# Performance work log

Hardware: AMD Instinct MI355X
Metric: run time of the kernel (lower is better)

## Reference

```python
import jax, jax.numpy as jnp
import numpy as np

BN_EPS = 1e-5
B, L, D = 16, 2048, 1024
OS = 64          # attnList[0]
NC = 256         # candidates per sample
CLASS_NUM = 8921
LAB = 1024


def setup_inputs() -> dict:
    key = jax.random.key(0)
    ks = jax.random.split(key, 8)
    scale_a = 1.0 / np.sqrt(D)
    return {
        "X": jax.random.normal(ks[0], (B, L, D), jnp.float32),
        "candidate": jax.random.randint(ks[1], (B, NC), 0, CLASS_NUM, jnp.int64),
        "a_w": jax.random.normal(ks[2], (D, OS), jnp.float32) * scale_a,
        "a_b": jnp.zeros((OS,), jnp.float32),
        "h_w": jax.random.normal(ks[3], (D, LAB), jnp.float32) * scale_a,
        "h_b": jnp.zeros((LAB,), jnp.float32),
        "bn_gamma": jax.random.uniform(ks[4], (LAB,), jnp.float32, 0.5, 1.5),
        "bn_beta": jax.random.normal(ks[5], (LAB,), jnp.float32) * 0.1,
        "bn_mean": jnp.zeros((LAB,), jnp.float32),
        "bn_var": jnp.ones((LAB,), jnp.float32),
        "labDescVec": jax.random.normal(ks[6], (CLASS_NUM, LAB), jnp.float32),
    }


def reference(X, candidate, a_w, a_b, h_w, h_b, bn_gamma, bn_beta, bn_mean, bn_var, labDescVec):
    # --- attention-pooling layer (attnList has one entry) ---
    # alpha: softmax over the sequence dim (dim=1 in torch)
    alpha = jax.nn.softmax(jnp.einsum('bld,do->blo', X, a_w) + a_b, axis=1)  # [B,L,OS]
    Xp = jnp.einsum('blo,bld->bod', alpha, X)                                # [B,OS,D]
    Xp = jnp.einsum('bod,dh->boh', Xp, h_w) + h_b                            # [B,OS,LAB]
    # BatchNorm1d over feature dim (eval mode: running stats)
    Xp = (Xp - bn_mean) * (bn_gamma / jnp.sqrt(bn_var + BN_EPS)) + bn_beta
    Xp = jax.nn.relu(Xp)  # dropout is identity at inference
    # --- candidate attention ---
    batchLabelVec = labDescVec[candidate]                                    # [B,NC,LAB]
    scores = jnp.einsum('boh,bch->boc', Xp, batchLabelVec)                   # [B,OS,NC]
    alpha2 = jax.nn.softmax(scores, axis=1)                                  # softmax over OS (dim=1)
    out = jnp.einsum('boc,boh->bch', alpha2, Xp)                             # [B,NC,LAB]
    return out
```

## Files before the change

kernel.cpp:

```cpp
#include <hip/hip_runtime.h>
#include <math.h>

#define Bb   16
#define Ll   2048
#define Dd   1024
#define OSo  64
#define NCc  256
#define LABh 1024
#define BN_EPS 1e-5f

typedef short s8v  __attribute__((ext_vector_type(8)));
typedef short s4v  __attribute__((ext_vector_type(4)));
typedef float f32x4 __attribute__((ext_vector_type(4)));

__device__ __forceinline__ short f2b(float f) {
    union { float f; unsigned u; } v; v.f = f;
    unsigned r = (v.u + 0x7fffu + ((v.u >> 16) & 1u)) >> 16;
    return (short)r;
}
__device__ __forceinline__ float b2f(short s) {
    union { unsigned u; float f; } v; v.u = ((unsigned)(unsigned short)s) << 16;
    return v.f;
}
__device__ __forceinline__ int swi(int row, int kElem) {
    return (row * 128 + ((kElem * 2) ^ ((row & 7) << 4))) >> 1;
}
__device__ __forceinline__ f32x4 MF(s8v a, s8v b, f32x4 c) {
    return __builtin_amdgcn_mfma_f32_16x16x32_bf16(a, b, c, 0, 0, 0);
}

__global__ __launch_bounds__(256) void k0(const float* __restrict__ h_w,
                                          const float* __restrict__ a_w,
                                          short* __restrict__ h_wT,
                                          short* __restrict__ a_wT) {
    __shared__ float t[64][68];
    const int tid = threadIdx.x, id = blockIdx.x;
    const float* src; short* dst; int srw, d0, y0;
    if (id < 256) { src = h_w; dst = h_wT; srw = LABh; d0 = (id & 15) * 64; y0 = (id >> 4) * 64; }
    else          { src = a_w; dst = a_wT; srw = OSo;  d0 = (id - 256) * 64; y0 = 0; }
    const int r = tid >> 2, cofs = (tid & 3) * 16;
    #pragma unroll
    for (int w = 0; w < 4; ++w) {
        float4 v = *(const float4*)&src[(size_t)(d0 + r) * srw + y0 + cofs + w * 4];
        t[r][cofs + w * 4 + 0] = v.x;
        t[r][cofs + w * 4 + 1] = v.y;
        t[r][cofs + w * 4 + 2] = v.z;
        t[r][cofs + w * 4 + 3] = v.w;
    }
    __syncthreads();
    s8v o0, o1;
    #pragma unroll
    for (int e = 0; e < 8; ++e) { o0[e] = f2b(t[cofs + e][r]); o1[e] = f2b(t[cofs + 8 + e][r]); }
    *(s8v*)&dst[(size_t)(y0 + r) * Dd + d0 + cofs]     = o0;
    *(s8v*)&dst[(size_t)(y0 + r) * Dd + d0 + cofs + 8] = o1;
}

struct R1 { float4 x[4]; s8v w[2]; };

__global__ __launch_bounds__(256) void k1(const float* __restrict__ X,
                                          const short* __restrict__ a_wT,
                                          const float* __restrict__ a_b,
                                          float* __restrict__ St) {
    __shared__ __align__(16) char smem[32768];
    float (*ts)[65] = (float(*)[65])smem;
    const int tid = threadIdx.x;
    const int lane = tid & 63, wave = tid >> 6;
    const int wm = wave >> 1, wn = wave & 1;
    const int b = blockIdx.y, l0 = blockIdx.x * 64;
    const float* Xb = X + ((size_t)b * Ll + l0) * Dd;
    const int r = tid >> 2, kofs = (tid & 3) * 16;
    f32x4 acc[2][2] = {};
    R1 cur, nxt;
    #pragma unroll
    for (int w = 0; w < 2; ++w) {
        cur.x[2*w]   = *(const float4*)&Xb[(size_t)r * Dd + kofs + w * 8];
        cur.x[2*w+1] = *(const float4*)&Xb[(size_t)r * Dd + kofs + w * 8 + 4];
        cur.w[w]     = *(const s8v*)&a_wT[(size_t)r * Dd + kofs + w * 8];
    }
    #pragma unroll
    for (int t = 0; t < 16; ++t) {
        short* As = (short*)(smem + (t & 1) * 8192);
        short* Bs = (short*)(smem + 16384 + (t & 1) * 8192);
        #pragma unroll
        for (int w = 0; w < 2; ++w) {
            const float* f0 = (const float*)&cur.x[2*w];
            s8v s;
            s[0]=f2b(f0[0]); s[1]=f2b(f0[1]); s[2]=f2b(f0[2]); s[3]=f2b(f0[3]);
            s[4]=f2b(f0[4]); s[5]=f2b(f0[5]); s[6]=f2b(f0[6]); s[7]=f2b(f0[7]);
            *(s8v*)&As[swi(r, kofs + w * 8)] = s;
            *(s8v*)&Bs[swi(r, kofs + w * 8)] = cur.w[w];
        }
        __syncthreads();
        if (t < 15) {
            const int k0 = (t + 1) * 64;
            #pragma unroll
            for (int w = 0; w < 2; ++w) {
                nxt.x[2*w]   = *(const float4*)&Xb[(size_t)r * Dd + k0 + kofs + w * 8];
                nxt.x[2*w+1] = *(const float4*)&Xb[(size_t)r * Dd + k0 + kofs + w * 8 + 4];
                nxt.w[w]     = *(const s8v*)&a_wT[(size_t)r * Dd + k0 + kofs + w * 8];
            }
        }
        #pragma unroll
        for (int kk = 0; kk < 2; ++kk) {
            const int kb = kk * 32 + (lane >> 4) * 8;
            s8v a[2], bb[2];
            #pragma unroll
            for (int i = 0; i < 2; ++i)
                a[i] = *(const s8v*)&As[swi(wm * 32 + i * 16 + (lane & 15), kb)];
            #pragma unroll
            for (int j = 0; j < 2; ++j)
                bb[j] = *(const s8v*)&Bs[swi(wn * 32 + j * 16 + (lane & 15), kb)];
            #pragma unroll
            for (int i = 0; i < 2; ++i)
                #pragma unroll
                for (int j = 0; j < 2; ++j)
                    acc[i][j] = MF(a[i], bb[j], acc[i][j]);
        }
        if (t < 15) cur = nxt;
    }
    __syncthreads();
    #pragma unroll
    for (int i = 0; i < 2; ++i)
        #pragma unroll
        for (int j = 0; j < 2; ++j)
            #pragma unroll
            for (int rr = 0; rr < 4; ++rr)
                ts[wm * 32 + i * 16 + (lane >> 4) * 4 + rr][wn * 32 + j * 16 + (lane & 15)] = acc[i][j][rr];
    __syncthreads();
    const int o = tid >> 2, lofs = (tid & 3) * 16;
    const float bias = a_b[o];
    float* Sp = St + ((size_t)b * OSo + o) * Ll + l0 + lofs;
    #pragma unroll
    for (int w = 0; w < 4; ++w) {
        float4 v;
        v.x = ts[lofs + w * 4 + 0][o] + bias;
        v.y = ts[lofs + w * 4 + 1][o] + bias;
        v.z = ts[lofs + w * 4 + 2][o] + bias;
        v.w = ts[lofs + w * 4 + 3][o] + bias;
        *(float4*)&Sp[w * 4] = v;
    }
}

__global__ __launch_bounds__(256) void k2(const float* __restrict__ St, short* __restrict__ aBf) {
    __shared__ float row[Ll];
    __shared__ float red[8];
    const float* p = St + (size_t)blockIdx.x * Ll;
    short* ab = aBf + (size_t)blockIdx.x * Ll;
    const int tid = threadIdx.x;
    const int wave = tid >> 6, lane = tid & 63;
    float m = -1e30f;
    for (int i = tid; i < Ll; i += 256) { float v = p[i]; row[i] = v; m = fmaxf(m, v); }
    #pragma unroll
    for (int off = 32; off; off >>= 1) m = fmaxf(m, __shfl_down(m, off));
    if (lane == 0) red[wave] = m;
    __syncthreads();
    if (tid == 0) red[4] = fmaxf(fmaxf(red[0], red[1]), fmaxf(red[2], red[3]));
    __syncthreads();
    const float M = red[4];
    float s = 0.f;
    for (int i = tid; i < Ll; i += 256) { float e = __expf(row[i] - M); row[i] = e; s += e; }
    __syncthreads();
    #pragma unroll
    for (int off = 32; off; off >>= 1) s += __shfl_down(s, off);
    if (lane == 0) red[wave] = s;
    __syncthreads();
    if (tid == 0) red[4] = 1.f / (red[0] + red[1] + red[2] + red[3]);
    __syncthreads();
    const float inv = red[4];
    for (int i = tid; i < Ll; i += 256) ab[i] = f2b(row[i] * inv);
}

struct R3 { s8v al[2]; float4 xv[4]; };

__global__ __launch_bounds__(256) void k3(const float* __restrict__ X,
                                          const short* __restrict__ aBf,
                                          float* __restrict__ XpP) {
    __shared__ __align__(16) char smem[32768];
    float (*ts)[68] = (float(*)[68])smem;
    const int tid = threadIdx.x;
    const int lane = tid & 63, wave = tid >> 6;
    const int wm = wave >> 1, wn = wave & 1;
    const int id = blockIdx.x;
    const int slot = id >> 3;
    const int b = (id & 7) * 2 + (slot >> 5);
    const int inner = slot & 31;
    const int dt = inner & 15, z = inner >> 4;
    const int d0 = dt * 64;
    const float* Xb = X + (size_t)b * Ll * Dd;
    const short* ab = aBf + (size_t)b * OSo * Ll;
    float* outP = XpP + (size_t)z * ((size_t)Bb * OSo * Dd);
    f32x4 acc[2][2] = {};
    const int arow = tid >> 2, akofs = (tid & 3) * 16;
    const int lq = tid & 15, dq = tid >> 4;
    const int lbase = z * 1024;
    R3 cur, nxt;
    #pragma unroll
    for (int w = 0; w < 2; ++w)
        cur.al[w] = *(const s8v*)&ab[(size_t)arow * Ll + lbase + akofs + w * 8];
    #pragma unroll
    for (int i = 0; i < 4; ++i)
        cur.xv[i] = *(const float4*)&Xb[(size_t)(lbase + lq * 4 + i) * Dd + d0 + dq * 4];
    #pragma unroll
    for (int t = 0; t < 16; ++t) {
        short* Aal = (short*)(smem + (t & 1) * 8192);
        short* Xs  = (short*)(smem + 16384 + (t & 1) * 8192);
        #pragma unroll
        for (int w = 0; w < 2; ++w)
            *(s8v*)&Aal[swi(arow, akofs + w * 8)] = cur.al[w];
        {
            const float* f = (const float*)cur.xv;
            #pragma unroll
            for (int j = 0; j < 4; ++j) {
                const int rowd = dq * 4 + j;
                s4v sj;
                sj[0] = f2b(f[0 * 4 + j]);
                sj[1] = f2b(f[1 * 4 + j]);
                sj[2] = f2b(f[2 * 4 + j]);
                sj[3] = f2b(f[3 * 4 + j]);
                *(s4v*)&Xs[swi(rowd, lq * 4)] = sj;
            }
        }
        __syncthreads();
        if (t < 15) {
            const int l0 = lbase + (t + 1) * 64;
            #pragma unroll
            for (int w = 0; w < 2; ++w)
                nxt.al[w] = *(const s8v*)&ab[(size_t)arow * Ll + l0 + akofs + w * 8];
            #pragma unroll
            for (int i = 0; i < 4; ++i)
                nxt.xv[i] = *(const float4*)&Xb[(size_t)(l0 + lq * 4 + i) * Dd + d0 + dq * 4];
        }
        #pragma unroll
        for (int kk = 0; kk < 2; ++kk) {
            const int kb = kk * 32 + (lane >> 4) * 8;
            s8v a[2], bb[2];
            #pragma unroll
            for (int i = 0; i < 2; ++i)
                a[i] = *(const s8v*)&Aal[swi(wm * 32 + i * 16 + (lane & 15), kb)];
            #pragma unroll
            for (int j = 0; j < 2; ++j)
                bb[j] = *(const s8v*)&Xs[swi(wn * 32 + j * 16 + (lane & 15), kb)];
            #pragma unroll
            for (int i = 0; i < 2; ++i)
                #pragma unroll
                for (int j = 0; j < 2; ++j)
                    acc[i][j] = MF(a[i], bb[j], acc[i][j]);
        }
        if (t < 15) cur = nxt;
    }
    __syncthreads();
    #pragma unroll
    for (int i = 0; i < 2; ++i)
        #pragma unroll
        for (int j = 0; j < 2; ++j)
            #pragma unroll
            for (int rr = 0; rr < 4; ++rr)
                ts[wm * 32 + i * 16 + (lane >> 4) * 4 + rr][wn * 32 + j * 16 + (lane & 15)] = acc[i][j][rr];
    __syncthreads();
    const int o = tid >> 2, dofs = (tid & 3) * 16;
    float* op = outP + ((size_t)b * OSo + o) * Dd + d0 + dofs;
    #pragma unroll
    for (int w = 0; w < 4; ++w)
        *(float4*)&op[w * 4] = *(float4*)&ts[o][dofs + w * 4];
}

struct R4 { float4 p[8]; s8v w[2]; };

__global__ __launch_bounds__(256) void k4(const float* __restrict__ XpP,
                                          const short* __restrict__ h_wT,
                                          const float* __restrict__ h_b,
                                          const float* __restrict__ gamma,
                                          const float* __restrict__ beta,
                                          const float* __restrict__ mean,
                                          const float* __restrict__ var,
                                          short* __restrict__ Xh) {
    __shared__ __align__(16) char smem[32768];
    short* tsb = (short*)smem;
    const int tid = threadIdx.x, lane = tid & 63, wave = tid >> 6;
    const int wm = wave >> 1, wn = wave & 1;
    const int h0 = blockIdx.x * 64, m0 = blockIdx.y * 64;
    const int r = tid >> 2, kofs = (tid & 3) * 16;
    const size_t ZS = (size_t)Bb * OSo * Dd;
    f32x4 acc[2][2] = {};
    R4 cur, nxt;
    #pragma unroll
    for (int w = 0; w < 2; ++w) {
        const float* p0 = XpP + (size_t)(m0 + r) * Dd + kofs + w * 8;
        cur.p[w*4+0] = *(const float4*)&p0[0];
        cur.p[w*4+1] = *(const float4*)&p0[4];
        cur.p[w*4+2] = *(const float4*)&p0[ZS];
        cur.p[w*4+3] = *(const float4*)&p0[ZS + 4];
        cur.w[w]     = *(const s8v*)&h_wT[(size_t)(h0 + r) * Dd + kofs + w * 8];
    }
    #pragma unroll
    for (int t = 0; t < 16; ++t) {
        short* As = (short*)(smem + (t & 1) * 8192);
        short* Bs = (short*)(smem + 16384 + (t & 1) * 8192);
        #pragma unroll
        for (int w = 0; w < 2; ++w) {
            const float* f0 = (const float*)&cur.p[w*4];
            const float* f1 = (const float*)&cur.p[w*4+2];
            s8v s;
            #pragma unroll
            for (int e = 0; e < 8; ++e) s[e] = f2b(f0[e] + f1[e]);
            *(s8v*)&As[swi(r, kofs + w * 8)] = s;
            *(s8v*)&Bs[swi(r, kofs + w * 8)] = cur.w[w];
        }
        __syncthreads();
        if (t < 15) {
            const int k0 = (t + 1) * 64;
            #pragma unroll
            for (int w = 0; w < 2; ++w) {
                const float* p0 = XpP + (size_t)(m0 + r) * Dd + k0 + kofs + w * 8;
                nxt.p[w*4+0] = *(const float4*)&p0[0];
                nxt.p[w*4+1] = *(const float4*)&p0[4];
                nxt.p[w*4+2] = *(const float4*)&p0[ZS];
                nxt.p[w*4+3] = *(const float4*)&p0[ZS + 4];
                nxt.w[w]     = *(const s8v*)&h_wT[(size_t)(h0 + r) * Dd + k0 + kofs + w * 8];
            }
        }
        #pragma unroll
        for (int kk = 0; kk < 2; ++kk) {
            const int kb = kk * 32 + (lane >> 4) * 8;
            s8v a[2], bb[2];
            #pragma unroll
            for (int i = 0; i < 2; ++i)
                a[i] = *(const s8v*)&As[swi(wm * 32 + i * 16 + (lane & 15), kb)];
            #pragma unroll
            for (int j = 0; j < 2; ++j)
                bb[j] = *(const s8v*)&Bs[swi(wn * 32 + j * 16 + (lane & 15), kb)];
            #pragma unroll
            for (int i = 0; i < 2; ++i)
                #pragma unroll
                for (int j = 0; j < 2; ++j)
                    acc[i][j] = MF(a[i], bb[j], acc[i][j]);
        }
        if (t < 15) cur = nxt;
    }
    __syncthreads();
    #pragma unroll
    for (int j = 0; j < 2; ++j) {
        const int h = h0 + wn * 32 + j * 16 + (lane & 15);
        const float sc = gamma[h] * rsqrtf(var[h] + BN_EPS);
        const float of = (h_b[h] - mean[h]) * sc + beta[h];
        #pragma unroll
        for (int i = 0; i < 2; ++i)
            #pragma unroll
            for (int rr = 0; rr < 4; ++rr) {
                const int ml = wm * 32 + i * 16 + (lane >> 4) * 4 + rr;
                tsb[ml * 64 + wn * 32 + j * 16 + (lane & 15)] = f2b(fmaxf(0.f, acc[i][j][rr] * sc + of));
            }
    }
    __syncthreads();
    #pragma unroll
    for (int w = 0; w < 2; ++w)
        *(s8v*)&Xh[(size_t)(m0 + r) * LABh + h0 + kofs + w * 8] = *(const s8v*)&tsb[r * 64 + kofs + w * 8];
}

struct R5 { float4 ld[4]; s8v xh[2]; };

__global__ __launch_bounds__(256) void k5(const int* __restrict__ cand,
                                          const float* __restrict__ labD,
                                          const short* __restrict__ Xh,
                                          float* __restrict__ scP) {
    __shared__ __align__(16) char smem[33024];
    float (*ts)[68] = (float(*)[68])smem;
    int* cidx = (int*)(smem + 32768);
    const int tid = threadIdx.x, lane = tid & 63, wave = tid >> 6;
    const int wm = wave >> 1, wn = wave & 1;
    const int b = blockIdx.y;
    const int ct = blockIdx.x & 3, z = blockIdx.x >> 2;
    const int c0 = ct * 64;
    const int kbase = z * 256;
    if (tid < 64) cidx[tid] = cand[b * NCc + c0 + tid];
    __syncthreads();
    const int r = tid >> 2, kofs = (tid & 3) * 16;
    const int ci = cidx[r];
    const float* lrow = labD + (size_t)ci * LABh + kbase;
    const short* xrow = Xh + (size_t)(b * OSo + r) * LABh + kbase;
    f32x4 acc[2][2] = {};
    R5 cur, nxt;
    #pragma unroll
    for (int w = 0; w < 2; ++w) {
        cur.ld[2*w]   = *(const float4*)&lrow[kofs + w * 8];
        cur.ld[2*w+1] = *(const float4*)&lrow[kofs + w * 8 + 4];
        cur.xh[w]     = *(const s8v*)&xrow[kofs + w * 8];
    }
    #pragma unroll
    for (int t = 0; t < 4; ++t) {
        short* As = (short*)(smem + (t & 1) * 8192);
        short* Bs = (short*)(smem + 16384 + (t & 1) * 8192);
        #pragma unroll
        for (int w = 0; w < 2; ++w) {
            const float* f0 = (const float*)&cur.ld[2*w];
            s8v s;
            #pragma unroll
            for (int e = 0; e < 8; ++e) s[e] = f2b(f0[e]);
            *(s8v*)&As[swi(r, kofs + w * 8)] = s;
            *(s8v*)&Bs[swi(r, kofs + w * 8)] = cur.xh[w];
        }
        __syncthreads();
        if (t < 3) {
            const int k0 = (t + 1) * 64;
            #pragma unroll
            for (int w = 0; w < 2; ++w) {
                cur.ld[2*w];
                nxt.ld[2*w]   = *(const float4*)&lrow[k0 + kofs + w * 8];
                nxt.ld[2*w+1] = *(const float4*)&lrow[k0 + kofs + w * 8 + 4];
                nxt.xh[w]     = *(const s8v*)&xrow[k0 + kofs + w * 8];
            }
        }
        #pragma unroll
        for (int kk = 0; kk < 2; ++kk) {
            const int kb = kk * 32 + (lane >> 4) * 8;
            s8v a[2], bb[2];
            #pragma unroll
            for (int i = 0; i < 2; ++i)
                a[i] = *(const s8v*)&As[swi(wm * 32 + i * 16 + (lane & 15), kb)];
            #pragma unroll
            for (int j = 0; j < 2; ++j)
                bb[j] = *(const s8v*)&Bs[swi(wn * 32 + j * 16 + (lane & 15), kb)];
            #pragma unroll
            for (int i = 0; i < 2; ++i)
                #pragma unroll
                for (int j = 0; j < 2; ++j)
                    acc[i][j] = MF(a[i], bb[j], acc[i][j]);
        }
        if (t < 3) cur = nxt;
    }
    __syncthreads();
    #pragma unroll
    for (int i = 0; i < 2; ++i)
        #pragma unroll
        for (int j = 0; j < 2; ++j)
            #pragma unroll
            for (int rr = 0; rr < 4; ++rr)
                ts[wm * 32 + i * 16 + (lane >> 4) * 4 + rr][wn * 32 + j * 16 + (lane & 15)] = acc[i][j][rr];
    __syncthreads();
    const int oofs = (tid & 3) * 16;
    float* sp = scP + (size_t)z * ((size_t)Bb * NCc * OSo)
                    + ((size_t)b * NCc + c0 + r) * OSo + oofs;
    #pragma unroll
    for (int w = 0; w < 4; ++w)
        *(float4*)&sp[w * 4] = *(float4*)&ts[r][oofs + w * 4];
}

__global__ __launch_bounds__(256) void k6(const float* __restrict__ scP,
                                          const short* __restrict__ Xh,
                                          float* __restrict__ out) {
    __shared__ float al[16][64];
    const int tid = threadIdx.x;
    const int id = blockIdx.x;
    const int b = (id & 7) * 2 + ((id >> 3) >> 4);
    const int c0 = ((id >> 3) & 15) * 16;
    const size_t ZS = (size_t)Bb * NCc * OSo;
    {
        const int cl = tid >> 4, t16 = tid & 15;
        const float* srow = scP + ((size_t)b * NCc + c0 + cl) * OSo;
        float v[4];
        float m = -1e30f;
        #pragma unroll
        for (int j = 0; j < 4; ++j) {
            v[j] = srow[t16 + j * 16] + srow[ZS + t16 + j * 16]
                 + srow[2 * ZS + t16 + j * 16] + srow[3 * ZS + t16 + j * 16];
            m = fmaxf(m, v[j]);
        }
        #pragma unroll
        for (int off = 8; off; off >>= 1) m = fmaxf(m, __shfl_xor(m, off, 16));
        float s = 0.f;
        #pragma unroll
        for (int j = 0; j < 4; ++j) { v[j] = __expf(v[j] - m); s += v[j]; }
        #pragma unroll
        for (int off = 8; off; off >>= 1) s += __shfl_xor(s, off, 16);
        float inv = 1.f / s;
        #pragma unroll
        for (int j = 0; j < 4; ++j) al[cl][t16 + j * 16] = v[j] * inv;
    }
    __syncthreads();
    const short* xb = Xh + (size_t)b * OSo * LABh;
    float acc[16][4] = {};
    for (int o = 0; o < OSo; ++o) {
        s4v xv = *(const s4v*)&xb[(size_t)o * LABh + tid * 4];
        const float x0 = b2f(xv[0]), x1 = b2f(xv[1]), x2 = b2f(xv[2]), x3 = b2f(xv[3]);
        #pragma unroll
        for (int c = 0; c < 16; ++c) {
            const float w = al[c][o];
            acc[c][0] += w * x0; acc[c][1] += w * x1; acc[c][2] += w * x2; acc[c][3] += w * x3;
        }
    }
    #pragma unroll
    for (int c = 0; c < 16; ++c) {
        float4 v; v.x = acc[c][0]; v.y = acc[c][1]; v.z = acc[c][2]; v.w = acc[c][3];
        *(float4*)&out[((size_t)b * NCc + c0 + c) * LABh + tid * 4] = v;
    }
}

extern "C" void kernel_launch(void* const* d_in, const int* in_sizes, int n_in,
                              void* d_out, int out_size, void* d_ws, size_t ws_size,
                              hipStream_t stream) {
    (void)in_sizes; (void)n_in; (void)out_size; (void)ws_size;
    const float* X      = (const float*)d_in[0];
    const int*   cand   = (const int*)  d_in[1];
    const float* a_w    = (const float*)d_in[2];
    const float* a_b    = (const float*)d_in[3];
    const float* h_w    = (const float*)d_in[4];
    const float* h_b    = (const float*)d_in[5];
    const float* gamma  = (const float*)d_in[6];
    const float* beta   = (const float*)d_in[7];
    const float* mean   = (const float*)d_in[8];
    const float* var    = (const float*)d_in[9];
    const float* labDesc= (const float*)d_in[10];
    float* outp = (float*)d_out;

    char* ws = (char*)d_ws;
    float* St   = (float*)ws;
    float* XpP  = St;
    short* aBf  = (short*)(ws + ((size_t)8  << 20));
    short* Xh   = (short*)(ws + ((size_t)12 << 20));
    float* scP  = (float*)(ws + ((size_t)14 << 20));
    short* a_wT = (short*)(ws + ((size_t)18 << 20));
    short* h_wT = (short*)(ws + ((size_t)19 << 20));

    k0 <<<272,          256, 0, stream>>>(h_w, a_w, h_wT, a_wT);
    k1 <<<dim3(32, 16), 256, 0, stream>>>(X, a_wT, a_b, St);
    k2 <<<Bb * OSo,     256, 0, stream>>>(St, aBf);
    k3 <<<512,          256, 0, stream>>>(X, aBf, XpP);
    k4 <<<dim3(16, 16), 256, 0, stream>>>(XpP, h_wT, h_b, gamma, beta, mean, var, Xh);
    k5 <<<dim3(16, 16), 256, 0, stream>>>(cand, labDesc, Xh, scP);
    k6 <<<256,          256, 0, stream>>>(scP, Xh, outp);
}
```

Before: 112.0 us.

## Split k1 over K, emit bf16 X copy for k3, double k6 grid

k1 is split into two K halves across blockIdx.z, producing partial scores that k2 sums along with the bias. While converting X to bf16 for its MFMA, k1 also writes that bf16 copy to workspace, so k3 reads half the bytes and skips its own conversion. k6 now uses 8 candidates per block and 512 blocks for more parallelism. The trade is an extra 64MB bf16 write plus a second partial-score buffer in exchange for halving k3's read traffic.

```diff
diff --git a/kernel.cpp b/kernel.cpp
--- a/kernel.cpp
+++ b/kernel.cpp
@@ -59,26 +59,29 @@
 
 __global__ __launch_bounds__(256) void k1(const float* __restrict__ X,
                                           const short* __restrict__ a_wT,
-                                          const float* __restrict__ a_b,
-                                          float* __restrict__ St) {
+                                          float* __restrict__ StP,
+                                          short* __restrict__ Xbf) {
     __shared__ __align__(16) char smem[32768];
     float (*ts)[65] = (float(*)[65])smem;
     const int tid = threadIdx.x;
     const int lane = tid & 63, wave = tid >> 6;
     const int wm = wave >> 1, wn = wave & 1;
     const int b = blockIdx.y, l0 = blockIdx.x * 64;
+    const int z = blockIdx.z, kbase = z * 512;
     const float* Xb = X + ((size_t)b * Ll + l0) * Dd;
+    short* XbfRow = Xbf + ((size_t)b * Ll + l0) * Dd;
     const int r = tid >> 2, kofs = (tid & 3) * 16;
     f32x4 acc[2][2] = {};
     R1 cur, nxt;
     #pragma unroll
     for (int w = 0; w < 2; ++w) {
-        cur.x[2*w]   = *(const float4*)&Xb[(size_t)r * Dd + kofs + w * 8];
-        cur.x[2*w+1] = *(const float4*)&Xb[(size_t)r * Dd + kofs + w * 8 + 4];
-        cur.w[w]     = *(const s8v*)&a_wT[(size_t)r * Dd + kofs + w * 8];
-    }
-    #pragma unroll
-    for (int t = 0; t < 16; ++t) {
+        cur.x[2*w]   = *(const float4*)&Xb[(size_t)r * Dd + kbase + kofs + w * 8];
+        cur.x[2*w+1] = *(const float4*)&Xb[(size_t)r * Dd + kbase + kofs + w * 8 + 4];
+        cur.w[w]     = *(const s8v*)&a_wT[(size_t)r * Dd + kbase + kofs + w * 8];
+    }
+    #pragma unroll
+    for (int t = 0; t < 8; ++t) {
+        const int k0 = kbase + t * 64;
         short* As = (short*)(smem + (t & 1) * 8192);
         short* Bs = (short*)(smem + 16384 + (t & 1) * 8192);
         #pragma unroll
@@ -89,15 +92,16 @@
             s[4]=f2b(f0[4]); s[5]=f2b(f0[5]); s[6]=f2b(f0[6]); s[7]=f2b(f0[7]);
             *(s8v*)&As[swi(r, kofs + w * 8)] = s;
             *(s8v*)&Bs[swi(r, kofs + w * 8)] = cur.w[w];
+            *(s8v*)&XbfRow[(size_t)r * Dd + k0 + kofs + w * 8] = s;
         }
         __syncthreads();
-        if (t < 15) {
-            const int k0 = (t + 1) * 64;
+        if (t < 7) {
+            const int kn = k0 + 64;
             #pragma unroll
             for (int w = 0; w < 2; ++w) {
-                nxt.x[2*w]   = *(const float4*)&Xb[(size_t)r * Dd + k0 + kofs + w * 8];
-                nxt.x[2*w+1] = *(const float4*)&Xb[(size_t)r * Dd + k0 + kofs + w * 8 + 4];
-                nxt.w[w]     = *(const s8v*)&a_wT[(size_t)r * Dd + k0 + kofs + w * 8];
+                nxt.x[2*w]   = *(const float4*)&Xb[(size_t)r * Dd + kn + kofs + w * 8];
+                nxt.x[2*w+1] = *(const float4*)&Xb[(size_t)r * Dd + kn + kofs + w * 8 + 4];
+                nxt.w[w]     = *(const s8v*)&a_wT[(size_t)r * Dd + kn + kofs + w * 8];
             }
         }
         #pragma unroll
@@ -116,7 +120,7 @@
                 for (int j = 0; j < 2; ++j)
                     acc[i][j] = MF(a[i], bb[j], acc[i][j]);
         }
-        if (t < 15) cur = nxt;
+        if (t < 7) cur = nxt;
     }
     __syncthreads();
     #pragma unroll
@@ -128,28 +132,36 @@
                 ts[wm * 32 + i * 16 + (lane >> 4) * 4 + rr][wn * 32 + j * 16 + (lane & 15)] = acc[i][j][rr];
     __syncthreads();
     const int o = tid >> 2, lofs = (tid & 3) * 16;
-    const float bias = a_b[o];
-    float* Sp = St + ((size_t)b * OSo + o) * Ll + l0 + lofs;
+    float* Sp = StP + (size_t)z * ((size_t)Bb * OSo * Ll)
+                    + ((size_t)b * OSo + o) * Ll + l0 + lofs;
     #pragma unroll
     for (int w = 0; w < 4; ++w) {
         float4 v;
-        v.x = ts[lofs + w * 4 + 0][o] + bias;
-        v.y = ts[lofs + w * 4 + 1][o] + bias;
-        v.z = ts[lofs + w * 4 + 2][o] + bias;
-        v.w = ts[lofs + w * 4 + 3][o] + bias;
+        v.x = ts[lofs + w * 4 + 0][o];
+        v.y = ts[lofs + w * 4 + 1][o];
+        v.z = ts[lofs + w * 4 + 2][o];
+        v.w = ts[lofs + w * 4 + 3][o];
         *(float4*)&Sp[w * 4] = v;
     }
 }
 
-__global__ __launch_bounds__(256) void k2(const float* __restrict__ St, short* __restrict__ aBf) {
+__global__ __launch_bounds__(256) void k2(const float* __restrict__ StP,
+                                          const float* __restrict__ a_b,
+                                          short* __restrict__ aBf) {
     __shared__ float row[Ll];
     __shared__ float red[8];
-    const float* p = St + (size_t)blockIdx.x * Ll;
+    const size_t ZS = (size_t)Bb * OSo * Ll;
+    const float* p0 = StP + (size_t)blockIdx.x * Ll;
+    const float* p1 = p0 + ZS;
     short* ab = aBf + (size_t)blockIdx.x * Ll;
     const int tid = threadIdx.x;
     const int wave = tid >> 6, lane = tid & 63;
+    const float bias = a_b[blockIdx.x & (OSo - 1)];
     float m = -1e30f;
-    for (int i = tid; i < Ll; i += 256) { float v = p[i]; row[i] = v; m = fmaxf(m, v); }
+    for (int i = tid; i < Ll; i += 256) {
+        float v = p0[i] + p1[i] + bias;
+        row[i] = v; m = fmaxf(m, v);
+    }
     #pragma unroll
     for (int off = 32; off; off >>= 1) m = fmaxf(m, __shfl_down(m, off));
     if (lane == 0) red[wave] = m;
@@ -170,9 +182,9 @@
     for (int i = tid; i < Ll; i += 256) ab[i] = f2b(row[i] * inv);
 }
 
-struct R3 { s8v al[2]; float4 xv[4]; };
-
-__global__ __launch_bounds__(256) void k3(const float* __restrict__ X,
+struct R3 { s8v al[2]; s4v xv[4]; };
+
+__global__ __launch_bounds__(256) void k3(const short* __restrict__ Xbf,
                                           const short* __restrict__ aBf,
                                           float* __restrict__ XpP) {
     __shared__ __align__(16) char smem[32768];
@@ -186,7 +198,7 @@
     const int inner = slot & 31;
     const int dt = inner & 15, z = inner >> 4;
     const int d0 = dt * 64;
-    const float* Xb = X + (size_t)b * Ll * Dd;
+    const short* Xb = Xbf + (size_t)b * Ll * Dd;
     const short* ab = aBf + (size_t)b * OSo * Ll;
     float* outP = XpP + (size_t)z * ((size_t)Bb * OSo * Dd);
     f32x4 acc[2][2] = {};
@@ -199,7 +211,7 @@
         cur.al[w] = *(const s8v*)&ab[(size_t)arow * Ll + lbase + akofs + w * 8];
     #pragma unroll
     for (int i = 0; i < 4; ++i)
-        cur.xv[i] = *(const float4*)&Xb[(size_t)(lbase + lq * 4 + i) * Dd + d0 + dq * 4];
+        cur.xv[i] = *(const s4v*)&Xb[(size_t)(lbase + lq * 4 + i) * Dd + d0 + dq * 4];
     #pragma unroll
     for (int t = 0; t < 16; ++t) {
         short* Aal = (short*)(smem + (t & 1) * 8192);
@@ -207,18 +219,15 @@
         #pragma unroll
         for (int w = 0; w < 2; ++w)
             *(s8v*)&Aal[swi(arow, akofs + w * 8)] = cur.al[w];
-        {
-            const float* f = (const float*)cur.xv;
-            #pragma unroll
-            for (int j = 0; j < 4; ++j) {
-                const int rowd = dq * 4 + j;
-                s4v sj;
-                sj[0] = f2b(f[0 * 4 + j]);
-                sj[1] = f2b(f[1 * 4 + j]);
-                sj[2] = f2b(f[2 * 4 + j]);
-                sj[3] = f2b(f[3 * 4 + j]);
-                *(s4v*)&Xs[swi(rowd, lq * 4)] = sj;
-            }
+        #pragma unroll
+        for (int j = 0; j < 4; ++j) {
+            const int rowd = dq * 4 + j;
+            s4v sj;
+            sj[0] = cur.xv[0][j];
+            sj[1] = cur.xv[1][j];
+            sj[2] = cur.xv[2][j];
+            sj[3] = cur.xv[3][j];
+            *(s4v*)&Xs[swi(rowd, lq * 4)] = sj;
         }
         __syncthreads();
         if (t < 15) {
@@ -228,7 +237,7 @@
                 nxt.al[w] = *(const s8v*)&ab[(size_t)arow * Ll + l0 + akofs + w * 8];
             #pragma unroll
             for (int i = 0; i < 4; ++i)
-                nxt.xv[i] = *(const float4*)&Xb[(size_t)(l0 + lq * 4 + i) * Dd + d0 + dq * 4];
+                nxt.xv[i] = *(const s4v*)&Xb[(size_t)(l0 + lq * 4 + i) * Dd + d0 + dq * 4];
         }
         #pragma unroll
         for (int kk = 0; kk < 2; ++kk) {
@@ -404,7 +413,6 @@
             const int k0 = (t + 1) * 64;
             #pragma unroll
             for (int w = 0; w < 2; ++w) {
-                cur.ld[2*w];
                 nxt.ld[2*w]   = *(const float4*)&lrow[k0 + kofs + w * 8];
                 nxt.ld[2*w+1] = *(const float4*)&lrow[k0 + kofs + w * 8 + 4];
                 nxt.xh[w]     = *(const s8v*)&xrow[k0 + kofs + w * 8];
@@ -448,48 +456,49 @@
 __global__ __launch_bounds__(256) void k6(const float* __restrict__ scP,
                                           const short* __restrict__ Xh,
                                           float* __restrict__ out) {
-    __shared__ float al[16][64];
+    __shared__ float al[8][64];
     const int tid = threadIdx.x;
     const int id = blockIdx.x;
-    const int b = (id & 7) * 2 + ((id >> 3) >> 4);
-    const int c0 = ((id >> 3) & 15) * 16;
+    const int slot = id >> 3;
+    const int b = (id & 7) * 2 + (slot >> 5);
+    const int c0 = (slot & 31) * 8;
     const size_t ZS = (size_t)Bb * NCc * OSo;
     {
-        const int cl = tid >> 4, t16 = tid & 15;
+        const int cl = tid >> 5, t32 = tid & 31;
         const float* srow = scP + ((size_t)b * NCc + c0 + cl) * OSo;
-        float v[4];
+        float v[2];
         float m = -1e30f;
         #pragma unroll
-        for (int j = 0; j < 4; ++j) {
-            v[j] = srow[t16 + j * 16] + srow[ZS + t16 + j * 16]
-                 + srow[2 * ZS + t16 + j * 16] + srow[3 * ZS + t16 + j * 16];
+        for (int j = 0; j < 2; ++j) {
+            const int o = t32 + j * 32;
+            v[j] = srow[o] + srow[ZS + o] + srow[2 * ZS + o] + srow[3 * ZS + o];
             m = fmaxf(m, v[j]);
         }
         #pragma unroll
-        for (int off = 8; off; off >>= 1) m = fmaxf(m, __shfl_xor(m, off, 16));
+        for (int off = 16; off; off >>= 1) m = fmaxf(m, __shfl_xor(m, off, 32));
         float s = 0.f;
         #pragma unroll
-        for (int j = 0; j < 4; ++j) { v[j] = __expf(v[j] - m); s += v[j]; }
-        #pragma unroll
-        for (int off = 8; off; off >>= 1) s += __shfl_xor(s, off, 16);
+        for (int j = 0; j < 2; ++j) { v[j] = __expf(v[j] - m); s += v[j]; }
+        #pragma unroll
+        for (int off = 16; off; off >>= 1) s += __shfl_xor(s, off, 32);
         float inv = 1.f / s;
         #pragma unroll
-        for (int j = 0; j < 4; ++j) al[cl][t16 + j * 16] = v[j] * inv;
+        for (int j = 0; j < 2; ++j) al[cl][t32 + j * 32] = v[j] * inv;
     }
     __syncthreads();
     const short* xb = Xh + (size_t)b * OSo * LABh;
-    float acc[16][4] = {};
+    float acc[8][4] = {};
     for (int o = 0; o < OSo; ++o) {
         s4v xv = *(const s4v*)&xb[(size_t)o * LABh + tid * 4];
         const float x0 = b2f(xv[0]), x1 = b2f(xv[1]), x2 = b2f(xv[2]), x3 = b2f(xv[3]);
         #pragma unroll
-        for (int c = 0; c < 16; ++c) {
+        for (int c = 0; c < 8; ++c) {
             const float w = al[c][o];
             acc[c][0] += w * x0; acc[c][1] += w * x1; acc[c][2] += w * x2; acc[c][3] += w * x3;
         }
     }
     #pragma unroll
-    for (int c = 0; c < 16; ++c) {
+    for (int c = 0; c < 8; ++c) {
         float4 v; v.x = acc[c][0]; v.y = acc[c][1]; v.z = acc[c][2]; v.w = acc[c][3];
         *(float4*)&out[((size_t)b * NCc + c0 + c) * LABh + tid * 4] = v;
     }
@@ -513,19 +522,20 @@
     float* outp = (float*)d_out;
 
     char* ws = (char*)d_ws;
-    float* St   = (float*)ws;
-    float* XpP  = St;
-    short* aBf  = (short*)(ws + ((size_t)8  << 20));
-    short* Xh   = (short*)(ws + ((size_t)12 << 20));
-    float* scP  = (float*)(ws + ((size_t)14 << 20));
-    short* a_wT = (short*)(ws + ((size_t)18 << 20));
-    short* h_wT = (short*)(ws + ((size_t)19 << 20));
-
-    k0 <<<272,          256, 0, stream>>>(h_w, a_w, h_wT, a_wT);
-    k1 <<<dim3(32, 16), 256, 0, stream>>>(X, a_wT, a_b, St);
-    k2 <<<Bb * OSo,     256, 0, stream>>>(St, aBf);
-    k3 <<<512,          256, 0, stream>>>(X, aBf, XpP);
-    k4 <<<dim3(16, 16), 256, 0, stream>>>(XpP, h_wT, h_b, gamma, beta, mean, var, Xh);
-    k5 <<<dim3(16, 16), 256, 0, stream>>>(cand, labDesc, Xh, scP);
-    k6 <<<256,          256, 0, stream>>>(scP, Xh, outp);
-}
+    float* StP  = (float*)ws;
+    float* XpP  = (float*)ws;
+    short* aBf  = (short*)(ws + ((size_t)16 << 20));
+    short* Xbf  = (short*)(ws + ((size_t)20 << 20));
+    short* Xh   = (short*)(ws + ((size_t)84 << 20));
+    float* scP  = (float*)(ws + ((size_t)86 << 20));
+    short* a_wT = (short*)(ws + ((size_t)90 << 20));
+    short* h_wT = (short*)(ws + ((size_t)91 << 20));
+
+    k0 <<<272,              256, 0, stream>>>(h_w, a_w, h_wT, a_wT);
+    k1 <<<dim3(32, 16, 2),  256, 0, stream>>>(X, a_wT, StP, Xbf);
+    k2 <<<Bb * OSo,         256, 0, stream>>>(StP, a_b, aBf);
+    k3 <<<512,              256, 0, stream>>>(Xbf, aBf, XpP);
+    k4 <<<dim3(16, 16),     256, 0, stream>>>(XpP, h_wT, h_b, gamma, beta, mean, var, Xh);
+    k5 <<<dim3(16, 16),     256, 0, stream>>>(cand, labDesc, Xh, scP);
+    k6 <<<512,              256, 0, stream>>>(scP, Xh, outp);
+}
```

Measured after the change: 124.6 us. +11.2%, slower.
